# Optimization experiments

Measured on AMD Instinct MI355X. Metric: run time of the kernel, lower is better.

## Reference

```python
import jax, jax.numpy as jnp
import numpy as np

N_NODES = 100000
N_EDGES = 1600000
IN_C, HID_C, OUT_C = 128, 128, 64
N_LAYERS, K, ALPHA = 4, 10, 0.1
LN_EPS = 1e-5


def setup_inputs() -> dict:
    key = jax.random.key(0)
    k1, k2, k3, k4, k5 = jax.random.split(key, 5)
    x = jax.random.normal(k1, (N_NODES, IN_C), dtype=jnp.float32)
    edge_index = jax.random.randint(k2, (2, N_EDGES), 0, N_NODES, dtype=jnp.int64)
    edge_weight = jax.random.uniform(k3, (N_EDGES,), dtype=jnp.float32)
    # Learned parameters (torch Linear default init scale ~ 1/sqrt(fan_in))
    W_enc = jax.random.normal(k4, (HID_C, IN_C), dtype=jnp.float32) / np.sqrt(IN_C)
    W_dec = jax.random.normal(k5, (OUT_C, HID_C), dtype=jnp.float32) / np.sqrt(HID_C)
    gamma = jnp.ones((HID_C,), dtype=jnp.float32)
    beta = jnp.zeros((HID_C,), dtype=jnp.float32)
    return {"x": x, "edge_index": edge_index, "edge_weight": edge_weight,
            "W_enc": W_enc, "W_dec": W_dec, "gamma": gamma, "beta": beta}


def _layer_norm(z, gamma, beta):
    mu = jnp.mean(z, axis=-1, keepdims=True)
    var = jnp.mean(jnp.square(z - mu), axis=-1, keepdims=True)
    return gamma * (z - mu) * jax.lax.rsqrt(var + LN_EPS) + beta


def _appnp(h, src, dst, w):
    # K-step personalized-pagerank propagation; normalize=False -> raw edge_weight
    x0 = h
    def step(_, z):
        msg = z[src] * w[:, None]                       # [E, HID_C] gather + scale
        agg = jax.ops.segment_sum(msg, dst, num_segments=N_NODES)  # scatter-add
        return (1.0 - ALPHA) * agg + ALPHA * x0
    return jax.lax.fori_loop(0, K, step, h)


def reference(x, edge_index, edge_weight, W_enc, W_dec, gamma, beta):
    src, dst = edge_index[0], edge_index[1]  # message flows source -> target
    h = x @ W_enc.T
    h = jax.nn.gelu(_layer_norm(h, gamma, beta), approximate=False)
    for _ in range(N_LAYERS):
        h = jax.nn.gelu(_appnp(h, src, dst, edge_weight), approximate=False)
        h = _layer_norm(h, gamma, beta)
    out = h @ W_dec.T
    return jnp.squeeze(out)
```

## Files before the change

kernel.cpp:

```cpp
#include <hip/hip_runtime.h>
#include <math.h>

#define N_NODES 100000
#define N_EDGES 1600000
#define IN_C 128
#define HID_C 128
#define OUT_C 64
#define NLAYERS 4
#define KSTEPS 10
#define ALPHA 0.1f
#define LN_EPS 1e-5f

#define SCAN_N (N_NODES + 1)
#define SCAN_BLOCKS ((SCAN_N + 1023) / 1024)
#define EP_CAP 2400000

__device__ __forceinline__ float gelu_exact(float x) {
    return 0.5f * x * (1.0f + erff(x * 0.70710678118654752f));
}

__device__ __forceinline__ unsigned pack_bf16_rne(float a, float b) {
    unsigned ua = __float_as_uint(a);
    unsigned ub = __float_as_uint(b);
    ua = (ua + 0x7fffu + ((ua >> 16) & 1u)) >> 16;
    ub = (ub + 0x7fffu + ((ub >> 16) & 1u)) >> 16;
    return (ub << 16) | ua;
}
__device__ __forceinline__ float bf_lo(unsigned d) { return __uint_as_float(d << 16); }
__device__ __forceinline__ float bf_hi(unsigned d) { return __uint_as_float(d & 0xffff0000u); }

__global__ void count_k(const int* __restrict__ dst, int* __restrict__ counts) {
    int e = blockIdx.x * blockDim.x + threadIdx.x;
    if (e < N_EDGES) atomicAdd(&counts[dst[e]], 1);
}

__global__ __launch_bounds__(1024) void scan1_k(const int* __restrict__ counts,
                                                int* __restrict__ bsum) {
    __shared__ int s[1024];
    int i = blockIdx.x * 1024 + threadIdx.x;
    int c = 0;
    if (i < N_NODES) c = (counts[i] + 7) & ~7;
    s[threadIdx.x] = c;
    __syncthreads();
    for (int off = 512; off; off >>= 1) {
        if (threadIdx.x < off) s[threadIdx.x] += s[threadIdx.x + off];
        __syncthreads();
    }
    if (threadIdx.x == 0) bsum[blockIdx.x] = s[0];
}

__global__ void scan2_k(int* __restrict__ bsum) {
    __shared__ int s[128];
    int t = threadIdx.x;
    s[t] = (t < SCAN_BLOCKS) ? bsum[t] : 0;
    __syncthreads();
    for (int off = 1; off < 128; off <<= 1) {
        int v = (t >= off) ? s[t - off] : 0;
        __syncthreads();
        s[t] += v;
        __syncthreads();
    }
    if (t < SCAN_BLOCKS) bsum[t] = (t == 0) ? 0 : s[t - 1];
}

__global__ __launch_bounds__(1024) void scan3_k(const int* __restrict__ counts,
                                                const int* __restrict__ bsum,
                                                int* __restrict__ row_off,
                                                int* __restrict__ fill_pos) {
    __shared__ int s[1024];
    int i = blockIdx.x * 1024 + threadIdx.x;
    int c = 0;
    if (i < N_NODES) c = (counts[i] + 7) & ~7;
    s[threadIdx.x] = c;
    __syncthreads();
    for (int off = 1; off < 1024; off <<= 1) {
        int v = (threadIdx.x >= off) ? s[threadIdx.x - off] : 0;
        __syncthreads();
        s[threadIdx.x] += v;
        __syncthreads();
    }
    if (i <= N_NODES) {
        int excl = s[threadIdx.x] - c + bsum[blockIdx.x];
        row_off[i] = excl;
        fill_pos[i] = excl;
    }
}

__global__ void bucket_k(const int* __restrict__ src, const int* __restrict__ dst,
                         const float* __restrict__ w,
                         int* __restrict__ fill_pos, int2* __restrict__ ep) {
    int e = blockIdx.x * blockDim.x + threadIdx.x;
    if (e >= N_EDGES) return;
    int d = dst[e];
    int pos = atomicAdd(&fill_pos[d], 1);
    float ws = (1.0f - ALPHA) * w[e];
    ep[pos] = make_int2(src[e] << 6, __float_as_int(ws));
}

__global__ __launch_bounds__(1024) void encoder_k(
        const float* __restrict__ x, const float* __restrict__ Wenc,
        const float* __restrict__ gamma, const float* __restrict__ beta,
        unsigned* __restrict__ H) {
    __shared__ float WT[IN_C * 130];
    __shared__ float XS[16][512];
    for (int i = threadIdx.x; i < IN_C * HID_C; i += 1024) {
        int c = i >> 7, k = i & 127;
        WT[k * 130 + c] = Wenc[i];
    }
    __syncthreads();
    int lane = threadIdx.x & 63;
    int wid  = threadIdx.x >> 6;
    const float2* WT2 = (const float2*)WT;
    float2 gb = ((const float2*)gamma)[lane];
    float2 bb = ((const float2*)beta)[lane];
    int wstride = gridDim.x * 16;
    float* xs = XS[wid];
    for (int grp = blockIdx.x * 16 + wid; grp * 4 < N_NODES; grp += wstride) {
        int r0 = grp * 4;
        const float4* xr = (const float4*)(x + (size_t)r0 * IN_C);
        ((float4*)xs)[lane]      = xr[lane];
        ((float4*)xs)[64 + lane] = xr[64 + lane];
        __builtin_amdgcn_wave_barrier();
        float a0x = 0, a0y = 0, a1x = 0, a1y = 0;
        float a2x = 0, a2y = 0, a3x = 0, a3y = 0;
        const float4* xs4 = (const float4*)xs;
#pragma unroll 4
        for (int k4 = 0; k4 < 32; ++k4) {
            float4 xv0 = xs4[k4];
            float4 xv1 = xs4[32 + k4];
            float4 xv2 = xs4[64 + k4];
            float4 xv3 = xs4[96 + k4];
            int k = k4 * 4;
            float2 w0 = WT2[(k + 0) * 65 + lane];
            float2 w1 = WT2[(k + 1) * 65 + lane];
            float2 w2 = WT2[(k + 2) * 65 + lane];
            float2 w3 = WT2[(k + 3) * 65 + lane];
#define ENC_ROW(ax, ay, xv)                                      \
            ax = fmaf(xv.x, w0.x, ax); ay = fmaf(xv.x, w0.y, ay); \
            ax = fmaf(xv.y, w1.x, ax); ay = fmaf(xv.y, w1.y, ay); \
            ax = fmaf(xv.z, w2.x, ax); ay = fmaf(xv.z, w2.y, ay); \
            ax = fmaf(xv.w, w3.x, ax); ay = fmaf(xv.w, w3.y, ay);
            ENC_ROW(a0x, a0y, xv0)
            ENC_ROW(a1x, a1y, xv1)
            ENC_ROW(a2x, a2y, xv2)
            ENC_ROW(a3x, a3y, xv3)
#undef ENC_ROW
        }
        __builtin_amdgcn_wave_barrier();
#define ENC_EPI(ax, ay, row)                                               \
        {                                                                   \
            float sum = ax + ay;                                            \
            for (int off = 32; off; off >>= 1) sum += __shfl_xor(sum, off); \
            float mu = sum * (1.0f / 128.0f);                               \
            float d0 = ax - mu, d1 = ay - mu;                               \
            float vs = d0 * d0 + d1 * d1;                                   \
            for (int off = 32; off; off >>= 1) vs += __shfl_xor(vs, off);   \
            float inv = rsqrtf(vs * (1.0f / 128.0f) + LN_EPS);              \
            float o0 = gelu_exact(gb.x * d0 * inv + bb.x);                  \
            float o1 = gelu_exact(gb.y * d1 * inv + bb.y);                  \
            H[(size_t)(row)*64 + lane] = pack_bf16_rne(o0, o1);             \
        }
        ENC_EPI(a0x, a0y, r0)
        ENC_EPI(a1x, a1y, r0 + 1)
        ENC_EPI(a2x, a2y, r0 + 2)
        ENC_EPI(a3x, a3y, r0 + 3)
#undef ENC_EPI
    }
}

__global__ __launch_bounds__(256) void prop_k(
        const unsigned* __restrict__ zin, const unsigned* __restrict__ x0,
        const int* __restrict__ row_off, const int2* __restrict__ ep,
        unsigned* __restrict__ zout, int fuse_ln,
        const float* __restrict__ gamma, const float* __restrict__ beta) {
    int gw = (blockIdx.x * 256 + threadIdx.x) >> 6;
    if (gw >= N_NODES) return;
    int lane = threadIdx.x & 63;
    int s0 = row_off[gw];
    int s1 = row_off[gw + 1];
    unsigned xd = x0[(size_t)gw * 64 + lane];
    float sx = 0.f, sy = 0.f;
    for (int base = s0; base < s1; base += 64) {
        int cnt = min(64, s1 - base);
        int2 p = make_int2(0, 0);
        if (lane < cnt) p = ep[base + lane];
        for (int j = 0; j < cnt; j += 8) {
#define EDGE(k, ov, wv)                                                     \
            int   ov = __builtin_amdgcn_readlane(p.x, j + k);               \
            float wv = __uint_as_float(                                     \
                (unsigned)__builtin_amdgcn_readlane(p.y, j + k));
            EDGE(0, o0, w0) EDGE(1, o1, w1) EDGE(2, o2, w2) EDGE(3, o3, w3)
            EDGE(4, o4, w4) EDGE(5, o5, w5) EDGE(6, o6, w6) EDGE(7, o7, w7)
#undef EDGE
            unsigned d0 = zin[o0 + lane];
            unsigned d1 = zin[o1 + lane];
            unsigned d2 = zin[o2 + lane];
            unsigned d3 = zin[o3 + lane];
            unsigned d4 = zin[o4 + lane];
            unsigned d5 = zin[o5 + lane];
            unsigned d6 = zin[o6 + lane];
            unsigned d7 = zin[o7 + lane];
            sx = fmaf(w0, bf_lo(d0), sx); sy = fmaf(w0, bf_hi(d0), sy);
            sx = fmaf(w1, bf_lo(d1), sx); sy = fmaf(w1, bf_hi(d1), sy);
            sx = fmaf(w2, bf_lo(d2), sx); sy = fmaf(w2, bf_hi(d2), sy);
            sx = fmaf(w3, bf_lo(d3), sx); sy = fmaf(w3, bf_hi(d3), sy);
            sx = fmaf(w4, bf_lo(d4), sx); sy = fmaf(w4, bf_hi(d4), sy);
            sx = fmaf(w5, bf_lo(d5), sx); sy = fmaf(w5, bf_hi(d5), sy);
            sx = fmaf(w6, bf_lo(d6), sx); sy = fmaf(w6, bf_hi(d6), sy);
            sx = fmaf(w7, bf_lo(d7), sx); sy = fmaf(w7, bf_hi(d7), sy);
        }
    }
    float zx = fmaf(ALPHA, bf_lo(xd), sx);
    float zy = fmaf(ALPHA, bf_hi(xd), sy);
    unsigned od;
    if (fuse_ln) {
        float h0 = gelu_exact(zx);
        float h1 = gelu_exact(zy);
        float sum = h0 + h1;
        for (int off = 32; off; off >>= 1) sum += __shfl_xor(sum, off);
        float mu = sum * (1.0f / 128.0f);
        float d0 = h0 - mu, d1 = h1 - mu;
        float vs = d0 * d0 + d1 * d1;
        for (int off = 32; off; off >>= 1) vs += __shfl_xor(vs, off);
        float inv = rsqrtf(vs * (1.0f / 128.0f) + LN_EPS);
        float2 gb = ((const float2*)gamma)[lane];
        float2 bb = ((const float2*)beta)[lane];
        od = pack_bf16_rne(gb.x * d0 * inv + bb.x, gb.y * d1 * inv + bb.y);
    } else {
        od = pack_bf16_rne(zx, zy);
    }
    zout[(size_t)gw * 64 + lane] = od;
}

__global__ __launch_bounds__(1024) void decoder_k(
        const unsigned* __restrict__ H, const float* __restrict__ Wdec,
        float* __restrict__ out) {
    __shared__ float WT[HID_C * 65];
    __shared__ unsigned XS[16][256];
    for (int i = threadIdx.x; i < OUT_C * HID_C; i += 1024) {
        int o = i >> 7, k = i & 127;
        WT[k * 65 + o] = Wdec[i];
    }
    __syncthreads();
    int lane = threadIdx.x & 63;
    int wid  = threadIdx.x >> 6;
    int wstride = gridDim.x * 16;
    unsigned* xs = XS[wid];
    for (int grp = blockIdx.x * 16 + wid; grp * 4 < N_NODES; grp += wstride) {
        int r0 = grp * 4;
        const unsigned* hp = H + (size_t)r0 * 64;
        xs[lane]       = hp[lane];
        xs[64 + lane]  = hp[64 + lane];
        xs[128 + lane] = hp[128 + lane];
        xs[192 + lane] = hp[192 + lane];
        __builtin_amdgcn_wave_barrier();
        float a0 = 0, a1 = 0, a2 = 0, a3 = 0;
#pragma unroll 4
        for (int k2 = 0; k2 < 64; ++k2) {
            float w0 = WT[(2 * k2) * 65 + lane];
            float w1 = WT[(2 * k2 + 1) * 65 + lane];
            unsigned u0 = xs[k2];
            unsigned u1 = xs[64 + k2];
            unsigned u2 = xs[128 + k2];
            unsigned u3 = xs[192 + k2];
            a0 = fmaf(bf_lo(u0), w0, a0); a0 = fmaf(bf_hi(u0), w1, a0);
            a1 = fmaf(bf_lo(u1), w0, a1); a1 = fmaf(bf_hi(u1), w1, a1);
            a2 = fmaf(bf_lo(u2), w0, a2); a2 = fmaf(bf_hi(u2), w1, a2);
            a3 = fmaf(bf_lo(u3), w0, a3); a3 = fmaf(bf_hi(u3), w1, a3);
        }
        __builtin_amdgcn_wave_barrier();
        out[(size_t)r0 * OUT_C + lane]       = a0;
        out[(size_t)(r0 + 1) * OUT_C + lane] = a1;
        out[(size_t)(r0 + 2) * OUT_C + lane] = a2;
        out[(size_t)(r0 + 3) * OUT_C + lane] = a3;
    }
}

extern "C" void kernel_launch(void* const* d_in, const int* in_sizes, int n_in,
                              void* d_out, int out_size, void* d_ws, size_t ws_size,
                              hipStream_t stream) {
    const float* x     = (const float*)d_in[0];
    const int*   ei    = (const int*)d_in[1];
    const float* ew    = (const float*)d_in[2];
    const float* Wenc  = (const float*)d_in[3];
    const float* Wdec  = (const float*)d_in[4];
    const float* gamma = (const float*)d_in[5];
    const float* beta  = (const float*)d_in[6];
    float* out = (float*)d_out;

    const int* src = ei;
    const int* dst = ei + N_EDGES;

    char* p = (char*)d_ws;
    auto carve = [&](size_t bytes) -> void* {
        void* r = (void*)p;
        p += (bytes + 255) & ~(size_t)255;
        return r;
    };
    int*  counts  = (int*)carve(SCAN_N * sizeof(int));
    int*  fillpos = (int*)carve(SCAN_N * sizeof(int));
    int*  row_off = (int*)carve(SCAN_N * sizeof(int));
    int*  bsum    = (int*)carve(SCAN_BLOCKS * sizeof(int));
    int2* ep      = (int2*)carve((size_t)EP_CAP * sizeof(int2));
    unsigned* H  = (unsigned*)carve((size_t)N_NODES * 64 * sizeof(unsigned));
    unsigned* ZA = (unsigned*)carve((size_t)N_NODES * 64 * sizeof(unsigned));
    unsigned* ZB = (unsigned*)carve((size_t)N_NODES * 64 * sizeof(unsigned));

    hipMemsetAsync(counts, 0, SCAN_N * sizeof(int), stream);
    hipMemsetAsync(ep, 0, (size_t)EP_CAP * sizeof(int2), stream);
    count_k<<<(N_EDGES + 255) / 256, 256, 0, stream>>>(dst, counts);
    scan1_k<<<SCAN_BLOCKS, 1024, 0, stream>>>(counts, bsum);
    scan2_k<<<1, 128, 0, stream>>>(bsum);
    scan3_k<<<SCAN_BLOCKS, 1024, 0, stream>>>(counts, bsum, row_off, fillpos);
    bucket_k<<<(N_EDGES + 255) / 256, 256, 0, stream>>>(src, dst, ew, fillpos, ep);

    encoder_k<<<512, 1024, 0, stream>>>(x, Wenc, gamma, beta, H);

    const int prop_blocks = (N_NODES + 3) / 4;
    unsigned* bufs[2] = {ZA, ZB};
    for (int l = 0; l < NLAYERS; ++l) {
        const unsigned* zin = H;
        for (int k = 0; k < KSTEPS; ++k) {
            int last = (k == KSTEPS - 1);
            unsigned* zout = last ? H : bufs[k & 1];
            prop_k<<<prop_blocks, 256, 0, stream>>>(zin, H, row_off, ep, zout,
                                                    last, gamma, beta);
            zin = zout;
        }
    }

    decoder_k<<<512, 1024, 0, stream>>>(H, Wdec, out);
}
```

Measured before the change: 2.799 ms.

## Split edge bucketing into destination-range passes and unroll gather by sixteen

```diff
diff --git a/kernel.cpp b/kernel.cpp
--- a/kernel.cpp
+++ b/kernel.cpp
@@ -14,6 +14,8 @@
 #define SCAN_N (N_NODES + 1)
 #define SCAN_BLOCKS ((SCAN_N + 1023) / 1024)
 #define EP_CAP 2400000
+#define BUCKET_PASSES 8
+#define BUCKET_RANGE ((N_NODES + BUCKET_PASSES - 1) / BUCKET_PASSES)
 
 __device__ __forceinline__ float gelu_exact(float x) {
     return 0.5f * x * (1.0f + erff(x * 0.70710678118654752f));
@@ -88,10 +90,12 @@
 
 __global__ void bucket_k(const int* __restrict__ src, const int* __restrict__ dst,
                          const float* __restrict__ w,
-                         int* __restrict__ fill_pos, int2* __restrict__ ep) {
+                         int* __restrict__ fill_pos, int2* __restrict__ ep,
+                         int lo, int hi) {
     int e = blockIdx.x * blockDim.x + threadIdx.x;
     if (e >= N_EDGES) return;
     int d = dst[e];
+    if (d < lo || d >= hi) return;
     int pos = atomicAdd(&fill_pos[d], 1);
     float ws = (1.0f - ALPHA) * w[e];
     ep[pos] = make_int2(src[e] << 6, __float_as_int(ws));
@@ -184,14 +188,54 @@
         int cnt = min(64, s1 - base);
         int2 p = make_int2(0, 0);
         if (lane < cnt) p = ep[base + lane];
-        for (int j = 0; j < cnt; j += 8) {
+        int j = 0;
 #define EDGE(k, ov, wv)                                                     \
-            int   ov = __builtin_amdgcn_readlane(p.x, j + k);               \
-            float wv = __uint_as_float(                                     \
-                (unsigned)__builtin_amdgcn_readlane(p.y, j + k));
+        int   ov = __builtin_amdgcn_readlane(p.x, j + k);                   \
+        float wv = __uint_as_float(                                         \
+            (unsigned)__builtin_amdgcn_readlane(p.y, j + k));
+        for (; j + 16 <= cnt; j += 16) {
+            EDGE(0,  o0,  w0)  EDGE(1,  o1,  w1)  EDGE(2,  o2,  w2)
+            EDGE(3,  o3,  w3)  EDGE(4,  o4,  w4)  EDGE(5,  o5,  w5)
+            EDGE(6,  o6,  w6)  EDGE(7,  o7,  w7)  EDGE(8,  o8,  w8)
+            EDGE(9,  o9,  w9)  EDGE(10, o10, w10) EDGE(11, o11, w11)
+            EDGE(12, o12, w12) EDGE(13, o13, w13) EDGE(14, o14, w14)
+            EDGE(15, o15, w15)
+            unsigned d0  = zin[o0  + lane];
+            unsigned d1  = zin[o1  + lane];
+            unsigned d2  = zin[o2  + lane];
+            unsigned d3  = zin[o3  + lane];
+            unsigned d4  = zin[o4  + lane];
+            unsigned d5  = zin[o5  + lane];
+            unsigned d6  = zin[o6  + lane];
+            unsigned d7  = zin[o7  + lane];
+            unsigned d8  = zin[o8  + lane];
+            unsigned d9  = zin[o9  + lane];
+            unsigned d10 = zin[o10 + lane];
+            unsigned d11 = zin[o11 + lane];
+            unsigned d12 = zin[o12 + lane];
+            unsigned d13 = zin[o13 + lane];
+            unsigned d14 = zin[o14 + lane];
+            unsigned d15 = zin[o15 + lane];
+            sx = fmaf(w0,  bf_lo(d0),  sx); sy = fmaf(w0,  bf_hi(d0),  sy);
+            sx = fmaf(w1,  bf_lo(d1),  sx); sy = fmaf(w1,  bf_hi(d1),  sy);
+            sx = fmaf(w2,  bf_lo(d2),  sx); sy = fmaf(w2,  bf_hi(d2),  sy);
+            sx = fmaf(w3,  bf_lo(d3),  sx); sy = fmaf(w3,  bf_hi(d3),  sy);
+            sx = fmaf(w4,  bf_lo(d4),  sx); sy = fmaf(w4,  bf_hi(d4),  sy);
+            sx = fmaf(w5,  bf_lo(d5),  sx); sy = fmaf(w5,  bf_hi(d5),  sy);
+            sx = fmaf(w6,  bf_lo(d6),  sx); sy = fmaf(w6,  bf_hi(d6),  sy);
+            sx = fmaf(w7,  bf_lo(d7),  sx); sy = fmaf(w7,  bf_hi(d7),  sy);
+            sx = fmaf(w8,  bf_lo(d8),  sx); sy = fmaf(w8,  bf_hi(d8),  sy);
+            sx = fmaf(w9,  bf_lo(d9),  sx); sy = fmaf(w9,  bf_hi(d9),  sy);
+            sx = fmaf(w10, bf_lo(d10), sx); sy = fmaf(w10, bf_hi(d10), sy);
+            sx = fmaf(w11, bf_lo(d11), sx); sy = fmaf(w11, bf_hi(d11), sy);
+            sx = fmaf(w12, bf_lo(d12), sx); sy = fmaf(w12, bf_hi(d12), sy);
+            sx = fmaf(w13, bf_lo(d13), sx); sy = fmaf(w13, bf_hi(d13), sy);
+            sx = fmaf(w14, bf_lo(d14), sx); sy = fmaf(w14, bf_hi(d14), sy);
+            sx = fmaf(w15, bf_lo(d15), sx); sy = fmaf(w15, bf_hi(d15), sy);
+        }
+        if (j < cnt) {
             EDGE(0, o0, w0) EDGE(1, o1, w1) EDGE(2, o2, w2) EDGE(3, o3, w3)
             EDGE(4, o4, w4) EDGE(5, o5, w5) EDGE(6, o6, w6) EDGE(7, o7, w7)
-#undef EDGE
             unsigned d0 = zin[o0 + lane];
             unsigned d1 = zin[o1 + lane];
             unsigned d2 = zin[o2 + lane];
@@ -209,6 +253,7 @@
             sx = fmaf(w6, bf_lo(d6), sx); sy = fmaf(w6, bf_hi(d6), sy);
             sx = fmaf(w7, bf_lo(d7), sx); sy = fmaf(w7, bf_hi(d7), sy);
         }
+#undef EDGE
     }
     float zx = fmaf(ALPHA, bf_lo(xd), sx);
     float zy = fmaf(ALPHA, bf_hi(xd), sy);
@@ -312,7 +357,12 @@
     scan1_k<<<SCAN_BLOCKS, 1024, 0, stream>>>(counts, bsum);
     scan2_k<<<1, 128, 0, stream>>>(bsum);
     scan3_k<<<SCAN_BLOCKS, 1024, 0, stream>>>(counts, bsum, row_off, fillpos);
-    bucket_k<<<(N_EDGES + 255) / 256, 256, 0, stream>>>(src, dst, ew, fillpos, ep);
+    for (int pss = 0; pss < BUCKET_PASSES; ++pss) {
+        int lo = pss * BUCKET_RANGE;
+        int hi = min(N_NODES, lo + BUCKET_RANGE);
+        bucket_k<<<(N_EDGES + 255) / 256, 256, 0, stream>>>(src, dst, ew,
+                                                            fillpos, ep, lo, hi);
+    }
 
     encoder_k<<<512, 1024, 0, stream>>>(x, Wenc, gamma, beta, H);
 
```

Result: no change. 2.812 ms (+0.4%).
